# Kernel optimization log

Measured on AMD Instinct MI355X. Metric: run time of the kernel, lower is better.

Reference implementation:

```python
import jax, jax.numpy as jnp
import numpy as np

A, B, S, ADIM = 8, 8192, 128, 16   # n_agents, batch, state_dim, act_dim
H, HEADS = 512, 4                   # hidc, att_heads
D = H // HEADS                      # att_dim
EPS = 1e-5


def _ln(x):
    # LayerNorm over last dim, no affine (elementwise_affine=False), eps=1e-5
    m = jnp.mean(x, axis=-1, keepdims=True)
    v = jnp.var(x, axis=-1, keepdims=True)
    return (x - m) * jax.lax.rsqrt(v + EPS)


def setup_inputs() -> dict:
    key = jax.random.key(0)
    ks = jax.random.split(key, 16)
    sc = 0.02
    return {
        "states": jax.random.normal(ks[0], (A, B, S), jnp.float32),
        "actions": jax.random.normal(ks[1], (A, B, ADIM), jnp.float32),
        # per-agent state encoders (Encoder built with hidc in the source)
        "Ws_s": jax.random.normal(ks[2], (A, S, H), jnp.float32) * sc,
        "bs_s": jnp.zeros((A, H), jnp.float32),
        # per-agent state-action encoders
        "Ws_sa": jax.random.normal(ks[3], (A, S + ADIM, H), jnp.float32) * sc,
        "bs_sa": jnp.zeros((A, H), jnp.float32),
        # shared per-head key/value/selector projections
        "Wk": jax.random.normal(ks[4], (HEADS, H, D), jnp.float32) * sc,
        "Wv": jax.random.normal(ks[5], (HEADS, H, D), jnp.float32) * sc,
        "Wsel": jax.random.normal(ks[6], (HEADS, H, D), jnp.float32) * sc,
        "bsel": jnp.zeros((HEADS, D), jnp.float32),
        # per-agent critics: Linear(2H -> H), LeakyReLU, Linear(H -> ADIM)
        "Wc1": jax.random.normal(ks[7], (A, 2 * H, H), jnp.float32) * sc,
        "bc1": jnp.zeros((A, H), jnp.float32),
        "Wc2": jax.random.normal(ks[8], (A, H, ADIM), jnp.float32) * sc,
        "bc2": jnp.zeros((A, ADIM), jnp.float32),
    }


def reference(states, actions, Ws_s, bs_s, Ws_sa, bs_sa,
              Wk, Wv, Wsel, bsel, Wc1, bc1, Wc2, bc2):
    lrelu = jax.nn.leaky_relu  # slope 0.01 matches torch default

    # per-agent state encodings: [A,B,H]
    s_enc = lrelu(jnp.einsum('abs,ash->abh', _ln(states), Ws_s) + bs_s[:, None, :])

    # per-agent state-action encodings: [A,B,H]
    sa = jnp.concatenate([states, actions], axis=-1)
    sa_enc = lrelu(jnp.einsum('abs,ash->abh', _ln(sa), Ws_sa) + bs_sa[:, None, :])

    # per-head keys / values / selectors: [HEADS, A, B, D]
    keys = jnp.einsum('abh,khd->kabd', sa_enc, Wk)
    vals = jnp.einsum('abh,khd->kabd', sa_enc, Wv)
    sel = lrelu(jnp.einsum('abh,khd->kabd', sa_enc, Wsel) + bsel[:, None, None, :])

    # attention logits of agent i over agents j != i: [HEADS, A, A, B]
    logits = jnp.einsum('kibd,kjbd->kijb', sel, keys) / np.sqrt(D).astype(np.float32)
    self_mask = jnp.eye(A, dtype=bool)[None, :, :, None]
    w = jax.nn.softmax(jnp.where(self_mask, -jnp.inf, logits), axis=2)

    # attended values: [HEADS, A, B, D] -> concat heads -> [A, B, H]
    qvals = jnp.einsum('kijb,kjbd->kibd', w, vals)
    values = qvals.transpose(1, 2, 0, 3).reshape(A, B, H)

    # per-agent critics on concat(state_enc, attended values)
    cin = jnp.concatenate([s_enc, values], axis=-1)           # [A,B,2H]
    h1 = lrelu(jnp.einsum('abf,afh->abh', _ln(cin), Wc1) + bc1[:, None, :])
    all_qs = jnp.einsum('abh,aho->abo', h1, Wc2) + bc2[:, None, :]  # [A,B,ADIM]

    # Q of taken (argmax) action per agent: [A,B,1]
    idx = jnp.argmax(actions, axis=-1)
    q = jnp.take_along_axis(all_qs, idx[..., None], axis=-1)
    return q
```

## Files before the change

### kernel.cpp

```cpp
#include <hip/hip_runtime.h>
#include <hip/hip_bf16.h>
#include <math.h>


#define AN 8
#define BNB 8192
#define SN 128
#define ADN 16
#define HN 512
#define NHEADS 4
#define DN 128

typedef __hip_bfloat16 bf16;
typedef unsigned short u16;
typedef __attribute__((ext_vector_type(8))) short bf16x8;
typedef __attribute__((ext_vector_type(4))) float f32x4;

__device__ __forceinline__ float lrelu(float x){ return x > 0.f ? x : 0.01f*x; }
__device__ __forceinline__ float bflo(unsigned u){ return __uint_as_float(u << 16); }
__device__ __forceinline__ float bfhi(unsigned u){ return __uint_as_float(u & 0xffff0000u); }
__device__ __forceinline__ float bf2f(u16 u){ return __uint_as_float((unsigned)u << 16); }
__device__ __forceinline__ u16 f2bf(float v){
  union { bf16 h; u16 s; } cv; cv.h = __float2bfloat16(v); return cv.s;
}
__device__ __forceinline__ ushort4 f4bf(float4 v){
  ushort4 u; u.x=f2bf(v.x); u.y=f2bf(v.y); u.z=f2bf(v.z); u.w=f2bf(v.w); return u;
}

__device__ __forceinline__ void gload16(const u16* g, u16* l){
  __builtin_amdgcn_global_load_lds(
      (const __attribute__((address_space(1))) unsigned int*)(g),
      (__attribute__((address_space(3))) unsigned int*)(l), 16, 0, 0);
}

__global__ __launch_bounds__(256) void prep_kernel(
    const float* __restrict__ states, const float* __restrict__ actions,
    u16* __restrict__ sa_bf, float2* __restrict__ st_s, float2* __restrict__ st_sa,
    int* __restrict__ aip)
{
  const int lane = threadIdx.x & 63;
  const int r = blockIdx.x*4 + (threadIdx.x >> 6);
  float2 sv = ((const float2*)(states + (size_t)r*SN))[lane];
  float s1 = sv.x + sv.y, q1 = sv.x*sv.x + sv.y*sv.y;
  float2 av = make_float2(0.f, 0.f);
  if (lane < 8) av = ((const float2*)(actions + (size_t)r*ADN))[lane];
  float s2 = s1 + av.x + av.y, q2 = q1 + av.x*av.x + av.y*av.y;
  #pragma unroll
  for (int off=32; off; off>>=1){
    s1 += __shfl_xor(s1,off); q1 += __shfl_xor(q1,off);
    s2 += __shfl_xor(s2,off); q2 += __shfl_xor(q2,off);
  }
  float bv; int bi;
  if (lane < 8){
    if (av.x >= av.y){ bv = av.x; bi = 2*lane; } else { bv = av.y; bi = 2*lane+1; }
  } else { bv = -INFINITY; bi = 999; }
  #pragma unroll
  for (int off=1; off<8; off<<=1){
    float ov = __shfl_xor(bv, off); int oi = __shfl_xor(bi, off);
    if (ov > bv || (ov == bv && oi < bi)){ bv = ov; bi = oi; }
  }
  u16* row = sa_bf + (size_t)r*192;
  ushort2 p; p.x = f2bf(sv.x); p.y = f2bf(sv.y);
  *(ushort2*)(row + 2*lane) = p;
  if (lane < 8){
    ushort2 pa; pa.x = f2bf(av.x); pa.y = f2bf(av.y);
    *(ushort2*)(row + 128 + 2*lane) = pa;
  } else if (lane < 32){
    ushort2 z; z.x = 0; z.y = 0;
    *(ushort2*)(row + 128 + 2*lane) = z;
  }
  if (lane==0){
    float m1 = s1*(1.f/128.f), v1 = fmaxf(q1*(1.f/128.f)-m1*m1, 0.f);
    st_s[r] = make_float2(m1, rsqrtf(v1+1e-5f));
    float m2 = s2*(1.f/144.f), v2 = fmaxf(q2*(1.f/144.f)-m2*m2, 0.f);
    st_sa[r] = make_float2(m2, rsqrtf(v2+1e-5f));
    aip[r] = bi;
  }
}

__global__ __launch_bounds__(256) void transw_all_kernel(
    const float* __restrict__ Ws_s, const float* __restrict__ Ws_sa, const float* __restrict__ Wc1,
    const float* __restrict__ Wk, const float* __restrict__ Wv, const float* __restrict__ Wsel,
    u16* __restrict__ Wt_s, u16* __restrict__ Wt_sa, u16* __restrict__ Wt_c1, u16* __restrict__ Wt_p)
{
  __shared__ float t[32][33];
  int id = blockIdx.x;
  const float* in; u16* outp; int K, Kp; size_t zs; int gx;
  const int N = (id < 5376) ? 512 : 128;
  if (id < 512){            in=Ws_s;  outp=Wt_s;            K=128;  Kp=128;  zs=(size_t)512*128;  gx=4;  }
  else if (id < 1280){ id-=512;  in=Ws_sa; outp=Wt_sa;      K=144;  Kp=192;  zs=(size_t)512*192;  gx=6;  }
  else if (id < 5376){ id-=1280; in=Wc1;   outp=Wt_c1;      K=1024; Kp=1024; zs=(size_t)512*1024; gx=32; }
  else if (id < 5632){ id-=5376; in=Wk;    outp=Wt_p;            K=512; Kp=512; zs=(size_t)3*128*512; gx=16; }
  else if (id < 5888){ id-=5632; in=Wv;    outp=Wt_p+128*512;    K=512; Kp=512; zs=(size_t)3*128*512; gx=16; }
  else {               id-=5888; in=Wsel;  outp=Wt_p+2*128*512;  K=512; Kp=512; zs=(size_t)3*128*512; gx=16; }
  const int bx = id % gx; id /= gx;
  const int gy = N >> 5;
  const int by = id % gy;
  const int z  = id / gy;
  const int tx = threadIdx.x, ty = threadIdx.y;
  const int k0 = bx*32, n0 = by*32;
  const float* ip = in + (size_t)z*K*N;
  #pragma unroll
  for (int i=0;i<4;i++){
    int k = k0 + ty*4 + i;
    t[ty*4+i][tx] = (k < K) ? ip[(size_t)k*N + n0 + tx] : 0.f;
  }
  __syncthreads();
  u16* op = outp + (size_t)z*zs;
  #pragma unroll
  for (int i=0;i<4;i++){
    int n = n0 + ty*4 + i;
    op[(size_t)n*Kp + k0 + tx] = f2bf(t[tx][ty*4+i]);
  }
}

__global__ __launch_bounds__(256) void colsum_bf_kernel(
    const u16* __restrict__ Wt_s, const u16* __restrict__ Wt_sa, const u16* __restrict__ Wt_c1,
    float* __restrict__ cs_s, float* __restrict__ cs_sa, float* __restrict__ cs_c1)
{
  const int lane = threadIdx.x & 63;
  const int row = blockIdx.x*4 + (threadIdx.x >> 6);
  const int which = row >> 12; const int idx = row & 4095;
  const u16* W; int K; float* outp;
  if (which==0){ W = Wt_s;  K = 128;  outp = cs_s;  }
  else if (which==1){ W = Wt_sa; K = 192;  outp = cs_sa; }
  else { W = Wt_c1; K = 1024; outp = cs_c1; }
  const u16* p = W + (size_t)idx*K;
  float s = 0.f;
  for (int c = lane*8; c < K; c += 512){
    uint4 v = *(const uint4*)(p + c);
    const unsigned w4[4] = {v.x, v.y, v.z, v.w};
    #pragma unroll
    for (int t=0;t<4;t++) s += bflo(w4[t]) + bfhi(w4[t]);
  }
  #pragma unroll
  for (int off=32; off; off>>=1) s += __shfl_xor(s,off);
  if (lane==0) outp[idx] = s;
}

template<int MODE>
__global__ __launch_bounds__(256) void mfma_enc_kernel(
    const u16* __restrict__ Aa, const u16* __restrict__ Ab,
    const u16* __restrict__ Wt, const float* __restrict__ bias,
    const float2* __restrict__ stats, const float* __restrict__ csum,
    u16* __restrict__ outp,
    const float* __restrict__ Wc2, const float* __restrict__ bc2,
    const int* __restrict__ aip, float* __restrict__ qout)
{
  constexpr int K   = (MODE==0) ? 128 : (MODE==1 ? 192 : 1024);
  constexpr int LDA = (MODE==2) ? 512 : 192;
  constexpr int KP  = K;
  constexpr int SMEMN = (MODE==2) ? 20736 : 17408;
  __shared__ __align__(16) u16 smem[SMEMN];
  u16* As = smem;
  u16* Bs = smem + 8192;
  const int tid = threadIdx.x;
  const int w = tid>>6, lane = tid&63;
  const int wr = w>>1, wc = w&1;
  const int srow = lane>>3, skq = (lane&7)^srow;

  const int nwg = gridDim.x * gridDim.y;
  int id = blockIdx.y * gridDim.x + blockIdx.x;
  int swz = (id & 7) * (nwg >> 3) + (id >> 3);
  const int bx = swz % gridDim.x, by = swz / gridDim.x;

  const int m0 = by*128, n0c = bx*128;
  const int a = by >> 6;
  const u16* Wbase = Wt + (size_t)a*HN*KP;
  const int slotbase = (lane>>4) ^ (lane&7);
  f32x4 acc[4][4] = {};

  float* wc2l = nullptr; int* ail = nullptr;
  if constexpr (MODE==2){
    wc2l = (float*)(smem + 16384);
    ail  = (int*)(smem + 16384 + 4096);
    for (int e = tid; e < 2048; e += 256){
      const int aidx = e >> 7, col = e & 127;
      wc2l[e] = Wc2[((size_t)a*HN + n0c + col)*ADN + aidx];
    }
    if (tid < 128) ail[tid] = aip[m0 + tid];
  }

  for (int k0 = 0; k0 < K; k0 += 64){
    __syncthreads();
    const u16* asrc; int acol;
    if (MODE==2){ asrc = (k0 < 512) ? Aa : Ab; acol = k0 & 511; }
    else        { asrc = Aa; acol = k0; }
    #pragma unroll
    for (int t=0;t<4;t++){
      const int rr = w*32 + t*8;
      gload16(asrc  + (size_t)(m0  + rr + srow)*LDA + acol + skq*8, As + rr*64);
      gload16(Wbase + (size_t)(n0c + rr + srow)*KP  + k0   + skq*8, Bs + rr*64);
    }
    __syncthreads();
    #pragma unroll
    for (int ks=0; ks<2; ++ks){
      bf16x8 af[4], bv[4];
      const int so = ((slotbase ^ (ks<<2)))*8;
      #pragma unroll
      for (int mi=0;mi<4;mi++) af[mi] = *(const bf16x8*)&As[(wr*64+mi*16+(lane&15))*64 + so];
      #pragma unroll
      for (int ni=0;ni<4;ni++) bv[ni] = *(const bf16x8*)&Bs[(wc*64+ni*16+(lane&15))*64 + so];
      #pragma unroll
      for (int mi=0;mi<4;mi++)
        #pragma unroll
        for (int ni=0;ni<4;ni++)
          acc[mi][ni] = __builtin_amdgcn_mfma_f32_16x16x32_bf16(af[mi], bv[ni], acc[mi][ni], 0, 0, 0);
    }
  }

  __syncthreads();
  float csv[4], biv[4];
  #pragma unroll
  for (int ni=0;ni<4;ni++){
    const int col = n0c + wc*64 + ni*16 + (lane&15);
    csv[ni] = csum[a*HN + col];
    biv[ni] = bias[a*HN + col];
  }

  if constexpr (MODE==2){
    #pragma unroll
    for (int mi=0;mi<4;mi++){
      const int rbase = wr*64 + mi*16 + ((lane>>4)<<2);
      #pragma unroll
      for (int v=0; v<4; ++v){
        const int rl = rbase + v;
        const float2 st = stats[m0 + rl];
        const int aidx = ail[rl];
        float p = 0.f;
        #pragma unroll
        for (int ni=0;ni<4;ni++){
          const int coll = wc*64 + ni*16 + (lane&15);
          const float o = lrelu(st.y*(acc[mi][ni][v] - st.x*csv[ni]) + biv[ni]);
          p = fmaf(o, wc2l[aidx*128 + coll], p);
        }
        p += __shfl_xor(p,1); p += __shfl_xor(p,2);
        p += __shfl_xor(p,4); p += __shfl_xor(p,8);
        if ((lane&15)==0){
          if (n0c==0 && wc==0) p += bc2[a*ADN + aidx];
          atomicAdd(qout + m0 + rl, p);
        }
      }
    }
  } else {
    #pragma unroll
    for (int mi=0;mi<4;mi++){
      const int rl = wr*64 + mi*16 + ((lane>>4)<<2);
      #pragma unroll
      for (int v=0; v<4; ++v){
        const float2 st = stats[m0 + rl + v];
        #pragma unroll
        for (int ni=0;ni<4;ni++){
          const float o = lrelu(st.y*(acc[mi][ni][v] - st.x*csv[ni]) + biv[ni]);
          smem[(rl+v)*136 + wc*64 + ni*16 + (lane&15)] = f2bf(o);
        }
      }
    }
    __syncthreads();
    #pragma unroll
    for (int it=0; it<8; ++it){
      const int rl = it*16 + (tid>>4);
      const int ck = (tid&15)*8;
      const uint4 vv = *(const uint4*)&smem[rl*136 + ck];
      *(uint4*)(outp + (size_t)(m0+rl)*HN + n0c + ck) = vv;
    }
  }
}

__global__ __launch_bounds__(256) void mfma_proj_kernel(
    const u16* __restrict__ sa_enc, const u16* __restrict__ Wt_p,
    const float* __restrict__ bsel, u16* __restrict__ kvs, int head)
{
  __shared__ __align__(16) u16 smem[17408];
  u16* As = smem;
  u16* Bs = smem + 8192;
  const int tid = threadIdx.x;
  const int w = tid>>6, lane = tid&63;
  const int wr = w>>1, wc = w&1;
  const int srow = lane>>3, skq = (lane&7)^srow;

  const int nwg = gridDim.x * gridDim.y;
  int id = blockIdx.y * gridDim.x + blockIdx.x;
  int swz = (id & 7) * (nwg >> 3) + (id >> 3);
  const int t = swz % gridDim.x;
  const int m0 = (swz / gridDim.x) * 128;

  const u16* Wbase = Wt_p + (size_t)(head*3 + t)*DN*HN;
  const int slotbase = (lane>>4) ^ (lane&7);
  f32x4 acc[4][4] = {};

  for (int k0 = 0; k0 < HN; k0 += 64){
    __syncthreads();
    #pragma unroll
    for (int tt=0;tt<4;tt++){
      const int rr = w*32 + tt*8;
      gload16(sa_enc + (size_t)(m0 + rr + srow)*HN + k0 + skq*8, As + rr*64);
      gload16(Wbase  + (size_t)(rr + srow)*HN      + k0 + skq*8, Bs + rr*64);
    }
    __syncthreads();
    #pragma unroll
    for (int ks=0; ks<2; ++ks){
      bf16x8 af[4], bv[4];
      const int so = ((slotbase ^ (ks<<2)))*8;
      #pragma unroll
      for (int mi=0;mi<4;mi++) af[mi] = *(const bf16x8*)&As[(wr*64+mi*16+(lane&15))*64 + so];
      #pragma unroll
      for (int ni=0;ni<4;ni++) bv[ni] = *(const bf16x8*)&Bs[(wc*64+ni*16+(lane&15))*64 + so];
      #pragma unroll
      for (int mi=0;mi<4;mi++)
        #pragma unroll
        for (int ni=0;ni<4;ni++)
          acc[mi][ni] = __builtin_amdgcn_mfma_f32_16x16x32_bf16(af[mi], bv[ni], acc[mi][ni], 0, 0, 0);
    }
  }

  __syncthreads();
  const bool issel = (t == 2);
  float biv[4];
  #pragma unroll
  for (int ni=0;ni<4;ni++){
    const int col = wc*64 + ni*16 + (lane&15);
    biv[ni] = issel ? bsel[head*DN + col] : 0.f;
  }
  #pragma unroll
  for (int mi=0;mi<4;mi++){
    const int rl = wr*64 + mi*16 + ((lane>>4)<<2);
    #pragma unroll
    for (int v=0; v<4; ++v){
      #pragma unroll
      for (int ni=0;ni<4;ni++){
        float o = acc[mi][ni][v] + biv[ni];
        if (issel) o = lrelu(o);
        smem[(rl+v)*136 + wc*64 + ni*16 + (lane&15)] = f2bf(o);
      }
    }
  }
  __syncthreads();
  #pragma unroll
  for (int it=0; it<8; ++it){
    const int rl = it*16 + (tid>>4);
    const int ck = (tid&15)*8;
    const int r = m0 + rl;
    const int ar = r >> 13, b = r & (BNB-1);
    const uint4 vv = *(const uint4*)&smem[rl*136 + ck];
    *(uint4*)(kvs + (((size_t)t*BNB + b)*AN + ar)*DN + ck) = vv;
  }
}

__global__ __launch_bounds__(256) void attn_kernel(
    const u16* __restrict__ kvs, u16* __restrict__ values, int kh)
{
  __shared__ float lds[4][3232];
  const int lane = threadIdx.x & 63;
  const int wv   = threadIdx.x >> 6;
  float* selL = &lds[wv][0];
  float* keyL = &lds[wv][1056];
  float* valL = &lds[wv][2112];
  float* wL   = &lds[wv][3168];
  const int b = blockIdx.x*4 + wv;

  #pragma unroll
  for (int m=0;m<3;m++){
    const int t = (m==0) ? 2 : ((m==1) ? 0 : 1);
    float* dst = (m==0) ? selL : ((m==1) ? keyL : valL);
    const uint2* p = (const uint2*)(kvs + ((size_t)t*BNB + b)*(AN*DN));
    #pragma unroll
    for (int it=0; it<4; it++){
      uint2 u = p[it*64 + lane];
      int e = (it*64 + lane)*4;
      int j = e >> 7, d = e & 127;
      float4 f;
      f.x = bflo(u.x); f.y = bfhi(u.x); f.z = bflo(u.y); f.w = bfhi(u.y);
      *(float4*)&dst[j*132 + d] = f;
    }
  }
  __syncthreads();

  const int i = lane >> 3, j = lane & 7;
  float acc = 0.f;
  #pragma unroll 8
  for (int dq=0; dq<32; dq++){
    const float4 s4 = *(const float4*)&selL[i*132 + dq*4];
    const float4 k4 = *(const float4*)&keyL[j*132 + dq*4];
    acc += s4.x*k4.x + s4.y*k4.y + s4.z*k4.z + s4.w*k4.w;
  }
  float logit = acc * 0.08838834764831845f;
  if (i == j) logit = -INFINITY;
  float mx = logit;
  mx = fmaxf(mx, __shfl_xor(mx,1,8));
  mx = fmaxf(mx, __shfl_xor(mx,2,8));
  mx = fmaxf(mx, __shfl_xor(mx,4,8));
  const float e = __expf(logit - mx);
  float s = e;
  s += __shfl_xor(s,1,8);
  s += __shfl_xor(s,2,8);
  s += __shfl_xor(s,4,8);
  wL[i*8 + j] = e / s;
  __syncthreads();

  const int dq = lane & 7;
  float4 o[4];
  #pragma unroll
  for (int tt=0;tt<4;tt++) o[tt] = make_float4(0.f,0.f,0.f,0.f);
  #pragma unroll
  for (int jj=0;jj<8;jj++){
    const float wj = wL[i*8 + jj];
    #pragma unroll
    for (int tt=0;tt<4;tt++){
      const float4 v4 = *(const float4*)&valL[jj*132 + tt*32 + dq*4];
      o[tt].x += wj*v4.x; o[tt].y += wj*v4.y; o[tt].z += wj*v4.z; o[tt].w += wj*v4.w;
    }
  }
  u16* dst = values + ((size_t)i*BNB + b)*HN + kh*DN;
  #pragma unroll
  for (int tt=0;tt<4;tt++)
    *(ushort4*)(dst + tt*32 + dq*4) = f4bf(o[tt]);
}

__global__ __launch_bounds__(256) void stats_cin_kernel(
    const u16* __restrict__ s_enc, const u16* __restrict__ values, float2* __restrict__ st)
{
  const int lane = threadIdx.x & 63;
  const int r = blockIdx.x*4 + (threadIdx.x >> 6);
  const uint4* p1 = (const uint4*)(s_enc + (size_t)r*HN);
  const uint4* p2 = (const uint4*)(values + (size_t)r*HN);
  uint4 va = p1[lane];
  uint4 vb = p2[lane];
  float s=0.f, q=0.f;
  const unsigned wa[4] = {va.x, va.y, va.z, va.w};
  const unsigned wb[4] = {vb.x, vb.y, vb.z, vb.w};
  #pragma unroll
  for (int t=0;t<4;t++){
    float f0 = bflo(wa[t]), f1 = bfhi(wa[t]);
    float g0 = bflo(wb[t]), g1 = bfhi(wb[t]);
    s += f0+f1+g0+g1; q += f0*f0+f1*f1+g0*g0+g1*g1;
  }
  #pragma unroll
  for (int off=32; off; off>>=1){ s += __shfl_xor(s,off); q += __shfl_xor(q,off); }
  if (lane==0){
    float m = s*(1.f/1024.f); float v = fmaxf(q*(1.f/1024.f) - m*m, 0.f);
    st[r] = make_float2(m, rsqrtf(v + 1e-5f));
  }
}

extern "C" void kernel_launch(void* const* d_in, const int* in_sizes, int n_in,
                              void* d_out, int out_size, void* d_ws, size_t ws_size,
                              hipStream_t stream)
{
  (void)in_sizes; (void)n_in; (void)ws_size;
  const float* states  = (const float*)d_in[0];
  const float* actions = (const float*)d_in[1];
  const float* Ws_s    = (const float*)d_in[2];
  const float* bs_s    = (const float*)d_in[3];
  const float* Ws_sa   = (const float*)d_in[4];
  const float* bs_sa   = (const float*)d_in[5];
  const float* Wk      = (const float*)d_in[6];
  const float* Wv      = (const float*)d_in[7];
  const float* Wsel    = (const float*)d_in[8];
  const float* bsel    = (const float*)d_in[9];
  const float* Wc1     = (const float*)d_in[10];
  const float* bc1     = (const float*)d_in[11];
  const float* Wc2     = (const float*)d_in[12];
  const float* bc2     = (const float*)d_in[13];
  float* outp = (float*)d_out;

  char* ws = (char*)d_ws;
  size_t off = 0;
  auto alloc = [&](size_t n){ void* p = ws + off; off += (n + 255) & ~(size_t)255; return p; };
  u16*    slot1  = (u16*)   alloc((size_t)AN*BNB*HN*2);
  u16*    s_enc  = slot1;
  u16*    kvs    = slot1;
  u16*    sa_enc = (u16*)   alloc((size_t)AN*BNB*HN*2);
  u16*    values = (u16*)   alloc((size_t)AN*BNB*HN*2);
  u16*    sa_bf  = (u16*)   alloc((size_t)AN*BNB*192*2);
  u16*    Wt_s   = (u16*)   alloc((size_t)AN*HN*128*2);
  u16*    Wt_sa  = (u16*)   alloc((size_t)AN*HN*192*2);
  u16*    Wt_c1  = (u16*)   alloc((size_t)AN*HN*1024*2);
  u16*    Wt_p   = (u16*)   alloc((size_t)NHEADS*3*DN*HN*2);
  float2* st_s   = (float2*)alloc((size_t)AN*BNB*8);
  float2* st_sa  = (float2*)alloc((size_t)AN*BNB*8);
  float2* st_cin = (float2*)alloc((size_t)AN*BNB*8);
  float*  cs_s   = (float*) alloc((size_t)AN*HN*4);
  float*  cs_sa  = (float*) alloc((size_t)AN*HN*4);
  float*  cs_c1  = (float*) alloc((size_t)AN*HN*4);
  int*    aip    = (int*)   alloc((size_t)AN*BNB*4);

  hipMemsetAsync(d_out, 0, (size_t)out_size*4, stream);
  prep_kernel<<<dim3(AN*BNB/4), 256, 0, stream>>>(states, actions, sa_bf, st_s, st_sa, aip);
  transw_all_kernel<<<dim3(6144), dim3(32,8), 0, stream>>>(
      Ws_s, Ws_sa, Wc1, Wk, Wv, Wsel, Wt_s, Wt_sa, Wt_c1, Wt_p);
  colsum_bf_kernel<<<dim3(3*AN*HN/4), 256, 0, stream>>>(Wt_s, Wt_sa, Wt_c1, cs_s, cs_sa, cs_c1);

  mfma_enc_kernel<1><<<dim3(4,512), 256, 0, stream>>>(sa_bf, nullptr, Wt_sa, bs_sa, st_sa, cs_sa,
                                                      sa_enc, nullptr, nullptr, nullptr, nullptr);
  for (int kh = 0; kh < NHEADS; ++kh){
    mfma_proj_kernel<<<dim3(3,512), 256, 0, stream>>>(sa_enc, Wt_p, bsel, kvs, kh);
    attn_kernel<<<dim3(BNB/4), 256, 0, stream>>>(kvs, values, kh);
  }
  mfma_enc_kernel<0><<<dim3(4,512), 256, 0, stream>>>(sa_bf, nullptr, Wt_s, bs_s, st_s, cs_s,
                                                      s_enc, nullptr, nullptr, nullptr, nullptr);
  stats_cin_kernel<<<dim3(AN*BNB/4), 256, 0, stream>>>(s_enc, values, st_cin);
  mfma_enc_kernel<2><<<dim3(4,512), 256, 0, stream>>>(s_enc, values, Wt_c1, bc1, st_cin, cs_c1,
                                                      nullptr, Wc2, bc2, aip, outp);
}
```

Baseline: 471.7 us.

## Fuse per-head key/value/selector projection with attention in one kernel

Replaces the per-head loop of projection GEMM plus attention kernels (8 launches) with one kernel per 8-batch tile. Each block keeps its 64 sa_enc rows in registers as A fragments, computes K, V and selector for every head into LDS, then runs the masked softmax attention and writes values directly. This removes the global round trip of the kvs intermediate and the repeated sa_enc reloads. In exchange each block streams all projection weights through LDS with only 64 rows of M, so weight reuse per block is lower. It uses 64KB of LDS and a large register footprint, which may limit occupancy.

After: 619.8 us. 31.4% more time.

```diff
diff --git a/kernel.cpp b/kernel.cpp
--- a/kernel.cpp
+++ b/kernel.cpp
@@ -22,6 +22,9 @@
 __device__ __forceinline__ float bf2f(u16 u){ return __uint_as_float((unsigned)u << 16); }
 __device__ __forceinline__ u16 f2bf(float v){
   union { bf16 h; u16 s; } cv; cv.h = __float2bfloat16(v); return cv.s;
+}
+__device__ __forceinline__ unsigned pk2(float a, float b){
+  return (unsigned)f2bf(a) | ((unsigned)f2bf(b) << 16);
 }
 __device__ __forceinline__ ushort4 f4bf(float4 v){
   ushort4 u; u.x=f2bf(v.x); u.y=f2bf(v.y); u.z=f2bf(v.z); u.w=f2bf(v.w); return u;
@@ -267,154 +270,136 @@
   }
 }
 
-__global__ __launch_bounds__(256) void mfma_proj_kernel(
+__global__ __launch_bounds__(256) void fused_pa_kernel(
     const u16* __restrict__ sa_enc, const u16* __restrict__ Wt_p,
-    const float* __restrict__ bsel, u16* __restrict__ kvs, int head)
-{
-  __shared__ __align__(16) u16 smem[17408];
-  u16* As = smem;
-  u16* Bs = smem + 8192;
+    const float* __restrict__ bsel, u16* __restrict__ values)
+{
+  __shared__ __align__(16) u16 smem[32768];
+  u16* Bst  = smem;
+  u16* bufK = smem + 8192;
+  u16* bufV = smem + 16384;
+  u16* bufS = smem + 24576;
   const int tid = threadIdx.x;
-  const int w = tid>>6, lane = tid&63;
-  const int wr = w>>1, wc = w&1;
-  const int srow = lane>>3, skq = (lane&7)^srow;
-
-  const int nwg = gridDim.x * gridDim.y;
-  int id = blockIdx.y * gridDim.x + blockIdx.x;
-  int swz = (id & 7) * (nwg >> 3) + (id >> 3);
-  const int t = swz % gridDim.x;
-  const int m0 = (swz / gridDim.x) * 128;
-
-  const u16* Wbase = Wt_p + (size_t)(head*3 + t)*DN*HN;
-  const int slotbase = (lane>>4) ^ (lane&7);
-  f32x4 acc[4][4] = {};
-
-  for (int k0 = 0; k0 < HN; k0 += 64){
+  const int w = tid >> 6, lane = tid & 63;
+  const int b0 = blockIdx.x * 8;
+  const int srow = lane >> 3, skq = (lane & 7) ^ srow;
+  const int slotbase = (lane >> 4) ^ (lane & 7);
+
+  bf16x8 af[16];
+  {
+    const int tr = lane & 15;
+    const int rr = w*16 + tr;
+    const u16* arow = sa_enc + ((size_t)(rr>>3)*BNB + b0 + (rr&7))*HN + (lane>>4)*8;
+    #pragma unroll
+    for (int kc = 0; kc < 16; ++kc)
+      af[kc] = *(const bf16x8*)(arow + kc*32);
+  }
+
+  for (int h = 0; h < NHEADS; ++h){
+    for (int t = 0; t < 3; ++t){
+      const u16* Wb = Wt_p + (size_t)(h*3 + t)*DN*HN;
+      f32x4 acc[8] = {};
+      #pragma unroll
+      for (int kc64 = 0; kc64 < 8; ++kc64){
+        __syncthreads();
+        #pragma unroll
+        for (int tt = 0; tt < 4; ++tt){
+          const int rb = w*32 + tt*8;
+          gload16(Wb + (size_t)(rb + srow)*HN + kc64*64 + skq*8, Bst + rb*64);
+        }
+        __syncthreads();
+        #pragma unroll
+        for (int ks = 0; ks < 2; ++ks){
+          const int so = (slotbase ^ (ks << 2)) * 8;
+          bf16x8 bv[8];
+          #pragma unroll
+          for (int ni = 0; ni < 8; ++ni)
+            bv[ni] = *(const bf16x8*)&Bst[(ni*16 + (lane & 15))*64 + so];
+          #pragma unroll
+          for (int ni = 0; ni < 8; ++ni)
+            acc[ni] = __builtin_amdgcn_mfma_f32_16x16x32_bf16(af[kc64*2+ks], bv[ni], acc[ni], 0, 0, 0);
+        }
+      }
+      u16* obuf = (t==0) ? bufK : (t==1) ? bufV : bufS;
+      float bsl[8];
+      if (t == 2){
+        #pragma unroll
+        for (int ni = 0; ni < 8; ++ni) bsl[ni] = bsel[h*DN + ni*16 + (lane&15)];
+      }
+      #pragma unroll
+      for (int ni = 0; ni < 8; ++ni){
+        #pragma unroll
+        for (int v = 0; v < 4; ++v){
+          const int rr2 = w*16 + ((lane>>4)<<2) + v;
+          float o = acc[ni][v];
+          if (t == 2) o = lrelu(o + bsl[ni]);
+          int idx = rr2*128 + ni*16 + (lane & 15);
+          idx ^= ((rr2 >> 3) & 7) << 3;
+          obuf[idx] = f2bf(o);
+        }
+      }
+    }
     __syncthreads();
-    #pragma unroll
-    for (int tt=0;tt<4;tt++){
-      const int rr = w*32 + tt*8;
-      gload16(sa_enc + (size_t)(m0 + rr + srow)*HN + k0 + skq*8, As + rr*64);
-      gload16(Wbase  + (size_t)(rr + srow)*HN      + k0 + skq*8, Bs + rr*64);
+
+    #pragma unroll
+    for (int bb = 0; bb < 2; ++bb){
+      const int i = w*2 + bb;
+      const int ai = lane >> 3, aj = lane & 7;
+      float dot = 0.f;
+      #pragma unroll
+      for (int s = 0; s < 16; ++s){
+        const int sidx = (ai*8 + i)*128 + ((s ^ ai) & 15)*8;
+        const int kidx = (aj*8 + i)*128 + ((s ^ aj) & 15)*8;
+        uint4 sv = *(const uint4*)&bufS[sidx];
+        uint4 kv = *(const uint4*)&bufK[kidx];
+        dot += bflo(sv.x)*bflo(kv.x) + bfhi(sv.x)*bfhi(kv.x);
+        dot += bflo(sv.y)*bflo(kv.y) + bfhi(sv.y)*bfhi(kv.y);
+        dot += bflo(sv.z)*bflo(kv.z) + bfhi(sv.z)*bfhi(kv.z);
+        dot += bflo(sv.w)*bflo(kv.w) + bfhi(sv.w)*bfhi(kv.w);
+      }
+      float logit = dot * 0.08838834764831845f;
+      if (ai == aj) logit = -INFINITY;
+      float mx = logit;
+      mx = fmaxf(mx, __shfl_xor(mx,1,8));
+      mx = fmaxf(mx, __shfl_xor(mx,2,8));
+      mx = fmaxf(mx, __shfl_xor(mx,4,8));
+      const float e = __expf(logit - mx);
+      float ssum = e;
+      ssum += __shfl_xor(ssum,1,8);
+      ssum += __shfl_xor(ssum,2,8);
+      ssum += __shfl_xor(ssum,4,8);
+      const float wgt = e / ssum;
+
+      const int dc = lane & 7;
+      float o[16];
+      #pragma unroll
+      for (int q = 0; q < 16; ++q) o[q] = 0.f;
+      #pragma unroll
+      for (int j = 0; j < 8; ++j){
+        const float wj = __shfl(wgt, j, 8);
+        const int vrow = (j*8 + i)*128;
+        const uint4 v0 = *(const uint4*)&bufV[vrow + (((dc*2)   ^ j) & 15)*8];
+        const uint4 v1 = *(const uint4*)&bufV[vrow + (((dc*2+1) ^ j) & 15)*8];
+        o[0]  += wj*bflo(v0.x); o[1]  += wj*bfhi(v0.x);
+        o[2]  += wj*bflo(v0.y); o[3]  += wj*bfhi(v0.y);
+        o[4]  += wj*bflo(v0.z); o[5]  += wj*bfhi(v0.z);
+        o[6]  += wj*bflo(v0.w); o[7]  += wj*bfhi(v0.w);
+        o[8]  += wj*bflo(v1.x); o[9]  += wj*bfhi(v1.x);
+        o[10] += wj*bflo(v1.y); o[11] += wj*bfhi(v1.y);
+        o[12] += wj*bflo(v1.z); o[13] += wj*bfhi(v1.z);
+        o[14] += wj*bflo(v1.w); o[15] += wj*bfhi(v1.w);
+      }
+      uint4 p0, p1;
+      p0.x = pk2(o[0],o[1]);   p0.y = pk2(o[2],o[3]);
+      p0.z = pk2(o[4],o[5]);   p0.w = pk2(o[6],o[7]);
+      p1.x = pk2(o[8],o[9]);   p1.y = pk2(o[10],o[11]);
+      p1.z = pk2(o[12],o[13]); p1.w = pk2(o[14],o[15]);
+      u16* dst = values + ((size_t)ai*BNB + b0 + i)*HN + h*DN + dc*16;
+      *(uint4*)dst = p0;
+      *(uint4*)(dst + 8) = p1;
     }
     __syncthreads();
-    #pragma unroll
-    for (int ks=0; ks<2; ++ks){
-      bf16x8 af[4], bv[4];
-      const int so = ((slotbase ^ (ks<<2)))*8;
-      #pragma unroll
-      for (int mi=0;mi<4;mi++) af[mi] = *(const bf16x8*)&As[(wr*64+mi*16+(lane&15))*64 + so];
-      #pragma unroll
-      for (int ni=0;ni<4;ni++) bv[ni] = *(const bf16x8*)&Bs[(wc*64+ni*16+(lane&15))*64 + so];
-      #pragma unroll
-      for (int mi=0;mi<4;mi++)
-        #pragma unroll
-        for (int ni=0;ni<4;ni++)
-          acc[mi][ni] = __builtin_amdgcn_mfma_f32_16x16x32_bf16(af[mi], bv[ni], acc[mi][ni], 0, 0, 0);
-    }
-  }
-
-  __syncthreads();
-  const bool issel = (t == 2);
-  float biv[4];
-  #pragma unroll
-  for (int ni=0;ni<4;ni++){
-    const int col = wc*64 + ni*16 + (lane&15);
-    biv[ni] = issel ? bsel[head*DN + col] : 0.f;
-  }
-  #pragma unroll
-  for (int mi=0;mi<4;mi++){
-    const int rl = wr*64 + mi*16 + ((lane>>4)<<2);
-    #pragma unroll
-    for (int v=0; v<4; ++v){
-      #pragma unroll
-      for (int ni=0;ni<4;ni++){
-        float o = acc[mi][ni][v] + biv[ni];
-        if (issel) o = lrelu(o);
-        smem[(rl+v)*136 + wc*64 + ni*16 + (lane&15)] = f2bf(o);
-      }
-    }
-  }
-  __syncthreads();
-  #pragma unroll
-  for (int it=0; it<8; ++it){
-    const int rl = it*16 + (tid>>4);
-    const int ck = (tid&15)*8;
-    const int r = m0 + rl;
-    const int ar = r >> 13, b = r & (BNB-1);
-    const uint4 vv = *(const uint4*)&smem[rl*136 + ck];
-    *(uint4*)(kvs + (((size_t)t*BNB + b)*AN + ar)*DN + ck) = vv;
-  }
-}
-
-__global__ __launch_bounds__(256) void attn_kernel(
-    const u16* __restrict__ kvs, u16* __restrict__ values, int kh)
-{
-  __shared__ float lds[4][3232];
-  const int lane = threadIdx.x & 63;
-  const int wv   = threadIdx.x >> 6;
-  float* selL = &lds[wv][0];
-  float* keyL = &lds[wv][1056];
-  float* valL = &lds[wv][2112];
-  float* wL   = &lds[wv][3168];
-  const int b = blockIdx.x*4 + wv;
-
-  #pragma unroll
-  for (int m=0;m<3;m++){
-    const int t = (m==0) ? 2 : ((m==1) ? 0 : 1);
-    float* dst = (m==0) ? selL : ((m==1) ? keyL : valL);
-    const uint2* p = (const uint2*)(kvs + ((size_t)t*BNB + b)*(AN*DN));
-    #pragma unroll
-    for (int it=0; it<4; it++){
-      uint2 u = p[it*64 + lane];
-      int e = (it*64 + lane)*4;
-      int j = e >> 7, d = e & 127;
-      float4 f;
-      f.x = bflo(u.x); f.y = bfhi(u.x); f.z = bflo(u.y); f.w = bfhi(u.y);
-      *(float4*)&dst[j*132 + d] = f;
-    }
-  }
-  __syncthreads();
-
-  const int i = lane >> 3, j = lane & 7;
-  float acc = 0.f;
-  #pragma unroll 8
-  for (int dq=0; dq<32; dq++){
-    const float4 s4 = *(const float4*)&selL[i*132 + dq*4];
-    const float4 k4 = *(const float4*)&keyL[j*132 + dq*4];
-    acc += s4.x*k4.x + s4.y*k4.y + s4.z*k4.z + s4.w*k4.w;
-  }
-  float logit = acc * 0.08838834764831845f;
-  if (i == j) logit = -INFINITY;
-  float mx = logit;
-  mx = fmaxf(mx, __shfl_xor(mx,1,8));
-  mx = fmaxf(mx, __shfl_xor(mx,2,8));
-  mx = fmaxf(mx, __shfl_xor(mx,4,8));
-  const float e = __expf(logit - mx);
-  float s = e;
-  s += __shfl_xor(s,1,8);
-  s += __shfl_xor(s,2,8);
-  s += __shfl_xor(s,4,8);
-  wL[i*8 + j] = e / s;
-  __syncthreads();
-
-  const int dq = lane & 7;
-  float4 o[4];
-  #pragma unroll
-  for (int tt=0;tt<4;tt++) o[tt] = make_float4(0.f,0.f,0.f,0.f);
-  #pragma unroll
-  for (int jj=0;jj<8;jj++){
-    const float wj = wL[i*8 + jj];
-    #pragma unroll
-    for (int tt=0;tt<4;tt++){
-      const float4 v4 = *(const float4*)&valL[jj*132 + tt*32 + dq*4];
-      o[tt].x += wj*v4.x; o[tt].y += wj*v4.y; o[tt].z += wj*v4.z; o[tt].w += wj*v4.w;
-    }
-  }
-  u16* dst = values + ((size_t)i*BNB + b)*HN + kh*DN;
-  #pragma unroll
-  for (int tt=0;tt<4;tt++)
-    *(ushort4*)(dst + tt*32 + dq*4) = f4bf(o[tt]);
+  }
 }
 
 __global__ __launch_bounds__(256) void stats_cin_kernel(
@@ -467,9 +452,7 @@
   char* ws = (char*)d_ws;
   size_t off = 0;
   auto alloc = [&](size_t n){ void* p = ws + off; off += (n + 255) & ~(size_t)255; return p; };
-  u16*    slot1  = (u16*)   alloc((size_t)AN*BNB*HN*2);
-  u16*    s_enc  = slot1;
-  u16*    kvs    = slot1;
+  u16*    s_enc  = (u16*)   alloc((size_t)AN*BNB*HN*2);
   u16*    sa_enc = (u16*)   alloc((size_t)AN*BNB*HN*2);
   u16*    values = (u16*)   alloc((size_t)AN*BNB*HN*2);
   u16*    sa_bf  = (u16*)   alloc((size_t)AN*BNB*192*2);
@@ -493,12 +476,9 @@
 
   mfma_enc_kernel<1><<<dim3(4,512), 256, 0, stream>>>(sa_bf, nullptr, Wt_sa, bs_sa, st_sa, cs_sa,
                                                       sa_enc, nullptr, nullptr, nullptr, nullptr);
-  for (int kh = 0; kh < NHEADS; ++kh){
-    mfma_proj_kernel<<<dim3(3,512), 256, 0, stream>>>(sa_enc, Wt_p, bsel, kvs, kh);
-    attn_kernel<<<dim3(BNB/4), 256, 0, stream>>>(kvs, values, kh);
-  }
   mfma_enc_kernel<0><<<dim3(4,512), 256, 0, stream>>>(sa_bf, nullptr, Wt_s, bs_s, st_s, cs_s,
                                                       s_enc, nullptr, nullptr, nullptr, nullptr);
+  fused_pa_kernel<<<dim3(BNB/8), 256, 0, stream>>>(sa_enc, Wt_p, bsel, values);
   stats_cin_kernel<<<dim3(AN*BNB/4), 256, 0, stream>>>(s_enc, values, st_cin);
   mfma_enc_kernel<2><<<dim3(4,512), 256, 0, stream>>>(s_enc, values, Wt_c1, bc1, st_cin, cs_c1,
                                                       nullptr, Wc2, bc2, aip, outp);
```

## Fuse critic LayerNorm statistics into encoder and attention epilogues via atomics

Applied to the files above, without the earlier changes.

Removes the separate stats_cin kernel that re-read s_enc and values to compute per-row mean and variance for the critic LayerNorm. The epilogues of the state encoder and of the attention kernel now accumulate each row's sum and sum of squares with atomics into a zeroed buffer. The critic kernel then derives mean and rstd from those sums. This saves a full pass over about 128 MB of bf16 data, at the cost of many float atomics and a memset. Statistics are now taken from fp32 values before bf16 rounding, which slightly changes numerics.

Measured after the change: 523.0 us. +10.9%, slower.

```diff
diff --git a/kernel.cpp b/kernel.cpp
--- a/kernel.cpp
+++ b/kernel.cpp
@@ -143,7 +143,7 @@
     const u16* __restrict__ Aa, const u16* __restrict__ Ab,
     const u16* __restrict__ Wt, const float* __restrict__ bias,
     const float2* __restrict__ stats, const float* __restrict__ csum,
-    u16* __restrict__ outp,
+    u16* __restrict__ outp, float2* __restrict__ stacc,
     const float* __restrict__ Wc2, const float* __restrict__ bc2,
     const int* __restrict__ aip, float* __restrict__ qout)
 {
@@ -225,13 +225,15 @@
       #pragma unroll
       for (int v=0; v<4; ++v){
         const int rl = rbase + v;
-        const float2 st = stats[m0 + rl];
+        const float2 sq = stats[m0 + rl];
+        const float mn = sq.x*(1.f/1024.f);
+        const float rstd = rsqrtf(fmaxf(sq.y*(1.f/1024.f) - mn*mn, 0.f) + 1e-5f);
         const int aidx = ail[rl];
         float p = 0.f;
         #pragma unroll
         for (int ni=0;ni<4;ni++){
           const int coll = wc*64 + ni*16 + (lane&15);
-          const float o = lrelu(st.y*(acc[mi][ni][v] - st.x*csv[ni]) + biv[ni]);
+          const float o = lrelu(rstd*(acc[mi][ni][v] - mn*csv[ni]) + biv[ni]);
           p = fmaf(o, wc2l[aidx*128 + coll], p);
         }
         p += __shfl_xor(p,1); p += __shfl_xor(p,2);
@@ -249,10 +251,22 @@
       #pragma unroll
       for (int v=0; v<4; ++v){
         const float2 st = stats[m0 + rl + v];
+        float rs = 0.f, rq = 0.f;
         #pragma unroll
         for (int ni=0;ni<4;ni++){
           const float o = lrelu(st.y*(acc[mi][ni][v] - st.x*csv[ni]) + biv[ni]);
           smem[(rl+v)*136 + wc*64 + ni*16 + (lane&15)] = f2bf(o);
+          rs += o; rq += o*o;
+        }
+        if constexpr (MODE==0){
+          rs += __shfl_xor(rs,1); rq += __shfl_xor(rq,1);
+          rs += __shfl_xor(rs,2); rq += __shfl_xor(rq,2);
+          rs += __shfl_xor(rs,4); rq += __shfl_xor(rq,4);
+          rs += __shfl_xor(rs,8); rq += __shfl_xor(rq,8);
+          if ((lane&15)==0){
+            float* sa = (float*)(stacc + m0 + rl + v);
+            atomicAdd(sa, rs); atomicAdd(sa+1, rq);
+          }
         }
       }
     }
@@ -348,7 +362,7 @@
 }
 
 __global__ __launch_bounds__(256) void attn_kernel(
-    const u16* __restrict__ kvs, u16* __restrict__ values, int kh)
+    const u16* __restrict__ kvs, u16* __restrict__ values, float2* __restrict__ stacc, int kh)
 {
   __shared__ float lds[4][3232];
   const int lane = threadIdx.x & 63;
@@ -415,31 +429,19 @@
   #pragma unroll
   for (int tt=0;tt<4;tt++)
     *(ushort4*)(dst + tt*32 + dq*4) = f4bf(o[tt]);
-}
-
-__global__ __launch_bounds__(256) void stats_cin_kernel(
-    const u16* __restrict__ s_enc, const u16* __restrict__ values, float2* __restrict__ st)
-{
-  const int lane = threadIdx.x & 63;
-  const int r = blockIdx.x*4 + (threadIdx.x >> 6);
-  const uint4* p1 = (const uint4*)(s_enc + (size_t)r*HN);
-  const uint4* p2 = (const uint4*)(values + (size_t)r*HN);
-  uint4 va = p1[lane];
-  uint4 vb = p2[lane];
-  float s=0.f, q=0.f;
-  const unsigned wa[4] = {va.x, va.y, va.z, va.w};
-  const unsigned wb[4] = {vb.x, vb.y, vb.z, vb.w};
-  #pragma unroll
-  for (int t=0;t<4;t++){
-    float f0 = bflo(wa[t]), f1 = bfhi(wa[t]);
-    float g0 = bflo(wb[t]), g1 = bfhi(wb[t]);
-    s += f0+f1+g0+g1; q += f0*f0+f1*f1+g0*g0+g1*g1;
-  }
-  #pragma unroll
-  for (int off=32; off; off>>=1){ s += __shfl_xor(s,off); q += __shfl_xor(q,off); }
-  if (lane==0){
-    float m = s*(1.f/1024.f); float v = fmaxf(q*(1.f/1024.f) - m*m, 0.f);
-    st[r] = make_float2(m, rsqrtf(v + 1e-5f));
+
+  float rs = 0.f, rq = 0.f;
+  #pragma unroll
+  for (int tt=0;tt<4;tt++){
+    rs += o[tt].x + o[tt].y + o[tt].z + o[tt].w;
+    rq += o[tt].x*o[tt].x + o[tt].y*o[tt].y + o[tt].z*o[tt].z + o[tt].w*o[tt].w;
+  }
+  rs += __shfl_xor(rs,1,8); rq += __shfl_xor(rq,1,8);
+  rs += __shfl_xor(rs,2,8); rq += __shfl_xor(rq,2,8);
+  rs += __shfl_xor(rs,4,8); rq += __shfl_xor(rq,4,8);
+  if (dq == 0){
+    float* sa = (float*)(stacc + (size_t)i*BNB + b);
+    atomicAdd(sa, rs); atomicAdd(sa + 1, rq);
   }
 }
 
@@ -486,20 +488,20 @@
   int*    aip    = (int*)   alloc((size_t)AN*BNB*4);
 
   hipMemsetAsync(d_out, 0, (size_t)out_size*4, stream);
+  hipMemsetAsync(st_cin, 0, (size_t)AN*BNB*8, stream);
   prep_kernel<<<dim3(AN*BNB/4), 256, 0, stream>>>(states, actions, sa_bf, st_s, st_sa, aip);
   transw_all_kernel<<<dim3(6144), dim3(32,8), 0, stream>>>(
       Ws_s, Ws_sa, Wc1, Wk, Wv, Wsel, Wt_s, Wt_sa, Wt_c1, Wt_p);
   colsum_bf_kernel<<<dim3(3*AN*HN/4), 256, 0, stream>>>(Wt_s, Wt_sa, Wt_c1, cs_s, cs_sa, cs_c1);
 
   mfma_enc_kernel<1><<<dim3(4,512), 256, 0, stream>>>(sa_bf, nullptr, Wt_sa, bs_sa, st_sa, cs_sa,
-                                                      sa_enc, nullptr, nullptr, nullptr, nullptr);
+                                                      sa_enc, nullptr, nullptr, nullptr, nullptr, nullptr);
   for (int kh = 0; kh < NHEADS; ++kh){
     mfma_proj_kernel<<<dim3(3,512), 256, 0, stream>>>(sa_enc, Wt_p, bsel, kvs, kh);
-    attn_kernel<<<dim3(BNB/4), 256, 0, stream>>>(kvs, values, kh);
+    attn_kernel<<<dim3(BNB/4), 256, 0, stream>>>(kvs, values, st_cin, kh);
   }
   mfma_enc_kernel<0><<<dim3(4,512), 256, 0, stream>>>(sa_bf, nullptr, Wt_s, bs_s, st_s, cs_s,
-                                                      s_enc, nullptr, nullptr, nullptr, nullptr);
-  stats_cin_kernel<<<dim3(AN*BNB/4), 256, 0, stream>>>(s_enc, values, st_cin);
+                                                      s_enc, st_cin, nullptr, nullptr, nullptr, nullptr);
   mfma_enc_kernel<2><<<dim3(4,512), 256, 0, stream>>>(s_enc, values, Wt_c1, bc1, st_cin, cs_c1,
-                                                      nullptr, Wc2, bc2, aip, outp);
-}
+                                                      nullptr, nullptr, Wc2, bc2, aip, outp);
+}
```

## Replace critic GEMM with 256x256-tile double-buffered pipelined MFMA kernel

Applied to the files above, without the earlier changes.

Splits the critic-layer GEMM (K=1024) out of the generic encoder kernel into a dedicated kernel. It uses 512 threads, 256x256 output tiles, and double-buffered LDS staging with async global loads interleaved between MFMA phases, plus explicit waitcnt, barriers and setprio. The aim is to hide global-load latency and raise arithmetic intensity on the largest GEMM, which the single-buffered 128x128 version left exposed. The larger LDS footprint (~148KB) and higher register pressure limit occupancy, and the hand scheduling is fragile.

Result: faster. 460.9 us (-2.3%).

```diff
diff --git a/kernel.cpp b/kernel.cpp
--- a/kernel.cpp
+++ b/kernel.cpp
@@ -140,18 +140,15 @@
 
 template<int MODE>
 __global__ __launch_bounds__(256) void mfma_enc_kernel(
-    const u16* __restrict__ Aa, const u16* __restrict__ Ab,
+    const u16* __restrict__ Aa,
     const u16* __restrict__ Wt, const float* __restrict__ bias,
     const float2* __restrict__ stats, const float* __restrict__ csum,
-    u16* __restrict__ outp,
-    const float* __restrict__ Wc2, const float* __restrict__ bc2,
-    const int* __restrict__ aip, float* __restrict__ qout)
-{
-  constexpr int K   = (MODE==0) ? 128 : (MODE==1 ? 192 : 1024);
-  constexpr int LDA = (MODE==2) ? 512 : 192;
+    u16* __restrict__ outp)
+{
+  constexpr int K   = (MODE==0) ? 128 : 192;
+  constexpr int LDA = 192;
   constexpr int KP  = K;
-  constexpr int SMEMN = (MODE==2) ? 20736 : 17408;
-  __shared__ __align__(16) u16 smem[SMEMN];
+  __shared__ __align__(16) u16 smem[17408];
   u16* As = smem;
   u16* Bs = smem + 8192;
   const int tid = threadIdx.x;
@@ -170,27 +167,13 @@
   const int slotbase = (lane>>4) ^ (lane&7);
   f32x4 acc[4][4] = {};
 
-  float* wc2l = nullptr; int* ail = nullptr;
-  if constexpr (MODE==2){
-    wc2l = (float*)(smem + 16384);
-    ail  = (int*)(smem + 16384 + 4096);
-    for (int e = tid; e < 2048; e += 256){
-      const int aidx = e >> 7, col = e & 127;
-      wc2l[e] = Wc2[((size_t)a*HN + n0c + col)*ADN + aidx];
-    }
-    if (tid < 128) ail[tid] = aip[m0 + tid];
-  }
-
   for (int k0 = 0; k0 < K; k0 += 64){
     __syncthreads();
-    const u16* asrc; int acol;
-    if (MODE==2){ asrc = (k0 < 512) ? Aa : Ab; acol = k0 & 511; }
-    else        { asrc = Aa; acol = k0; }
     #pragma unroll
     for (int t=0;t<4;t++){
       const int rr = w*32 + t*8;
-      gload16(asrc  + (size_t)(m0  + rr + srow)*LDA + acol + skq*8, As + rr*64);
-      gload16(Wbase + (size_t)(n0c + rr + srow)*KP  + k0   + skq*8, Bs + rr*64);
+      gload16(Aa    + (size_t)(m0  + rr + srow)*LDA + k0 + skq*8, As + rr*64);
+      gload16(Wbase + (size_t)(n0c + rr + srow)*KP  + k0 + skq*8, Bs + rr*64);
     }
     __syncthreads();
     #pragma unroll
@@ -217,52 +200,202 @@
     csv[ni] = csum[a*HN + col];
     biv[ni] = bias[a*HN + col];
   }
-
-  if constexpr (MODE==2){
-    #pragma unroll
-    for (int mi=0;mi<4;mi++){
-      const int rbase = wr*64 + mi*16 + ((lane>>4)<<2);
-      #pragma unroll
-      for (int v=0; v<4; ++v){
-        const int rl = rbase + v;
-        const float2 st = stats[m0 + rl];
-        const int aidx = ail[rl];
-        float p = 0.f;
-        #pragma unroll
-        for (int ni=0;ni<4;ni++){
-          const int coll = wc*64 + ni*16 + (lane&15);
-          const float o = lrelu(st.y*(acc[mi][ni][v] - st.x*csv[ni]) + biv[ni]);
-          p = fmaf(o, wc2l[aidx*128 + coll], p);
-        }
-        p += __shfl_xor(p,1); p += __shfl_xor(p,2);
-        p += __shfl_xor(p,4); p += __shfl_xor(p,8);
-        if ((lane&15)==0){
-          if (n0c==0 && wc==0) p += bc2[a*ADN + aidx];
-          atomicAdd(qout + m0 + rl, p);
-        }
-      }
-    }
-  } else {
-    #pragma unroll
-    for (int mi=0;mi<4;mi++){
-      const int rl = wr*64 + mi*16 + ((lane>>4)<<2);
-      #pragma unroll
-      for (int v=0; v<4; ++v){
-        const float2 st = stats[m0 + rl + v];
-        #pragma unroll
-        for (int ni=0;ni<4;ni++){
-          const float o = lrelu(st.y*(acc[mi][ni][v] - st.x*csv[ni]) + biv[ni]);
-          smem[(rl+v)*136 + wc*64 + ni*16 + (lane&15)] = f2bf(o);
-        }
-      }
-    }
-    __syncthreads();
-    #pragma unroll
-    for (int it=0; it<8; ++it){
-      const int rl = it*16 + (tid>>4);
-      const int ck = (tid&15)*8;
-      const uint4 vv = *(const uint4*)&smem[rl*136 + ck];
-      *(uint4*)(outp + (size_t)(m0+rl)*HN + n0c + ck) = vv;
+  #pragma unroll
+  for (int mi=0;mi<4;mi++){
+    const int rl = wr*64 + mi*16 + ((lane>>4)<<2);
+    #pragma unroll
+    for (int v=0; v<4; ++v){
+      const float2 st = stats[m0 + rl + v];
+      #pragma unroll
+      for (int ni=0;ni<4;ni++){
+        const float o = lrelu(st.y*(acc[mi][ni][v] - st.x*csv[ni]) + biv[ni]);
+        smem[(rl+v)*136 + wc*64 + ni*16 + (lane&15)] = f2bf(o);
+      }
+    }
+  }
+  __syncthreads();
+  #pragma unroll
+  for (int it=0; it<8; ++it){
+    const int rl = it*16 + (tid>>4);
+    const int ck = (tid&15)*8;
+    const uint4 vv = *(const uint4*)&smem[rl*136 + ck];
+    *(uint4*)(outp + (size_t)(m0+rl)*HN + n0c + ck) = vv;
+  }
+}
+
+__global__ __launch_bounds__(512, 2) void mfma_critic_kernel(
+    const u16* __restrict__ Aa, const u16* __restrict__ Ab,
+    const u16* __restrict__ Wt, const float* __restrict__ bias,
+    const float2* __restrict__ stats, const float* __restrict__ csum,
+    const float* __restrict__ Wc2, const float* __restrict__ bc2,
+    const int* __restrict__ aip, float* __restrict__ qout)
+{
+  __shared__ __align__(16) u16 smem[74240];
+  const int tid = threadIdx.x;
+  const int w = tid >> 6, lane = tid & 63;
+  const int wr = w >> 2, wc = w & 3;
+  const int srow = lane >> 3, skq = (lane & 7) ^ srow;
+  const int slotx = lane >> 4, lanx = lane & 7, lr = lane & 15;
+
+  const int nwg = gridDim.x * gridDim.y;
+  int id = blockIdx.y * gridDim.x + blockIdx.x;
+  int swz = (id & 7) * (nwg >> 3) + (id >> 3);
+  const int bx = swz % gridDim.x, by = swz / gridDim.x;
+  const int m0 = by * 256, n0c = bx * 256;
+  const int a = m0 >> 13;
+  const u16* Wbase = Wt + (size_t)a * HN * 1024;
+
+  float* wc2l = (float*)(smem + 65536);
+  int*   ail  = (int*)(smem + 65536 + 8192);
+  #pragma unroll
+  for (int i = 0; i < 8; ++i){
+    const int e = i*512 + tid;
+    const int aidx = e >> 8, col = e & 255;
+    wc2l[e] = Wc2[((size_t)a*HN + n0c + col)*ADN + aidx];
+  }
+  if (tid < 256) ail[tid] = aip[m0 + tid];
+
+  auto STAGE = [&](int tau, int part){
+    u16* dst = smem + (tau & 1)*32768 + ((part >> 1) ? 16384 : 0) + (part & 1)*8192 + w*1024;
+    if (part < 2){
+      const int k0 = tau * 64;
+      const u16* asrc = (k0 < 512) ? Aa : Ab;
+      const int acol = (k0 & 511) + skq*8;
+      const int grow = m0 + (part & 1)*128 + w*16 + srow;
+      gload16(asrc + (size_t)grow*HN + acol, dst);
+      gload16(asrc + (size_t)(grow + 8)*HN + acol, dst + 512);
+    } else {
+      const int bcol = tau*64 + skq*8;
+      const int grow = n0c + (part & 1)*128 + w*16 + srow;
+      gload16(Wbase + (size_t)grow*1024 + bcol, dst);
+      gload16(Wbase + (size_t)(grow + 8)*1024 + bcol, dst + 512);
+    }
+  };
+
+  STAGE(0,0); STAGE(0,1); STAGE(0,2); STAGE(0,3);
+  STAGE(1,0); STAGE(1,1); STAGE(1,2); STAGE(1,3);
+  asm volatile("s_waitcnt vmcnt(8)" ::: "memory");
+  __builtin_amdgcn_sched_barrier(0);
+  __builtin_amdgcn_s_barrier();
+
+  f32x4 acc[8][4] = {};
+
+  #pragma unroll 1
+  for (int tau = 0; tau < 16; ++tau){
+    const u16* AB = smem + (tau & 1)*32768;
+    const int so0 = ((0 | slotx) ^ lanx)*8;
+    const int so1 = ((4 | slotx) ^ lanx)*8;
+    bf16x8 af[4][2], bn01[2][2], bn23[2][2];
+
+    #pragma unroll
+    for (int mf = 0; mf < 4; ++mf){
+      const int r = (wr*128 + mf*16 + lr)*64;
+      af[mf][0] = *(const bf16x8*)&AB[r + so0];
+      af[mf][1] = *(const bf16x8*)&AB[r + so1];
+    }
+    #pragma unroll
+    for (int nf = 0; nf < 2; ++nf){
+      const int r = 16384 + (wc*64 + nf*16 + lr)*64;
+      bn01[nf][0] = *(const bf16x8*)&AB[r + so0];
+      bn01[nf][1] = *(const bf16x8*)&AB[r + so1];
+    }
+    if (tau >= 1 && tau <= 14) STAGE(tau + 1, 0);
+    __builtin_amdgcn_s_barrier();
+    __builtin_amdgcn_s_setprio(1);
+    #pragma unroll
+    for (int mf = 0; mf < 4; ++mf)
+      #pragma unroll
+      for (int nf = 0; nf < 2; ++nf){
+        acc[mf][nf] = __builtin_amdgcn_mfma_f32_16x16x32_bf16(af[mf][0], bn01[nf][0], acc[mf][nf], 0,0,0);
+        acc[mf][nf] = __builtin_amdgcn_mfma_f32_16x16x32_bf16(af[mf][1], bn01[nf][1], acc[mf][nf], 0,0,0);
+      }
+    __builtin_amdgcn_s_setprio(0);
+    __builtin_amdgcn_s_barrier();
+
+    #pragma unroll
+    for (int nf = 0; nf < 2; ++nf){
+      const int r = 16384 + (wc*64 + (nf + 2)*16 + lr)*64;
+      bn23[nf][0] = *(const bf16x8*)&AB[r + so0];
+      bn23[nf][1] = *(const bf16x8*)&AB[r + so1];
+    }
+    if (tau >= 1 && tau <= 14) STAGE(tau + 1, 1);
+    __builtin_amdgcn_s_barrier();
+    __builtin_amdgcn_s_setprio(1);
+    #pragma unroll
+    for (int mf = 0; mf < 4; ++mf)
+      #pragma unroll
+      for (int nf = 0; nf < 2; ++nf){
+        acc[mf][nf+2] = __builtin_amdgcn_mfma_f32_16x16x32_bf16(af[mf][0], bn23[nf][0], acc[mf][nf+2], 0,0,0);
+        acc[mf][nf+2] = __builtin_amdgcn_mfma_f32_16x16x32_bf16(af[mf][1], bn23[nf][1], acc[mf][nf+2], 0,0,0);
+      }
+    __builtin_amdgcn_s_setprio(0);
+    __builtin_amdgcn_s_barrier();
+
+    #pragma unroll
+    for (int mf = 0; mf < 4; ++mf){
+      const int r = (wr*128 + (mf + 4)*16 + lr)*64;
+      af[mf][0] = *(const bf16x8*)&AB[r + so0];
+      af[mf][1] = *(const bf16x8*)&AB[r + so1];
+    }
+    if (tau <= 13) STAGE(tau + 2, 2);
+    __builtin_amdgcn_s_barrier();
+    __builtin_amdgcn_s_setprio(1);
+    #pragma unroll
+    for (int mf = 0; mf < 4; ++mf)
+      #pragma unroll
+      for (int nf = 0; nf < 2; ++nf){
+        acc[mf+4][nf+2] = __builtin_amdgcn_mfma_f32_16x16x32_bf16(af[mf][0], bn23[nf][0], acc[mf+4][nf+2], 0,0,0);
+        acc[mf+4][nf+2] = __builtin_amdgcn_mfma_f32_16x16x32_bf16(af[mf][1], bn23[nf][1], acc[mf+4][nf+2], 0,0,0);
+      }
+    __builtin_amdgcn_s_setprio(0);
+    __builtin_amdgcn_s_barrier();
+
+    if (tau <= 13) STAGE(tau + 2, 3);
+    __builtin_amdgcn_s_barrier();
+    __builtin_amdgcn_s_setprio(1);
+    #pragma unroll
+    for (int mf = 0; mf < 4; ++mf)
+      #pragma unroll
+      for (int nf = 0; nf < 2; ++nf){
+        acc[mf+4][nf] = __builtin_amdgcn_mfma_f32_16x16x32_bf16(af[mf][0], bn01[nf][0], acc[mf+4][nf], 0,0,0);
+        acc[mf+4][nf] = __builtin_amdgcn_mfma_f32_16x16x32_bf16(af[mf][1], bn01[nf][1], acc[mf+4][nf], 0,0,0);
+      }
+    __builtin_amdgcn_s_setprio(0);
+
+    if (tau < 14)       { asm volatile("s_waitcnt vmcnt(4)" ::: "memory"); }
+    else if (tau == 14) { asm volatile("s_waitcnt vmcnt(0)" ::: "memory"); }
+    __builtin_amdgcn_sched_barrier(0);
+    __builtin_amdgcn_s_barrier();
+    __builtin_amdgcn_sched_barrier(0);
+  }
+
+  float csv[4], biv[4];
+  #pragma unroll
+  for (int nf = 0; nf < 4; ++nf){
+    const int col = n0c + wc*64 + nf*16 + lr;
+    csv[nf] = csum[a*HN + col];
+    biv[nf] = bias[a*HN + col];
+  }
+  #pragma unroll
+  for (int mf = 0; mf < 8; ++mf){
+    const int rbase = wr*128 + mf*16 + slotx*4;
+    #pragma unroll
+    for (int v = 0; v < 4; ++v){
+      const int rl = rbase + v;
+      const float2 st = stats[m0 + rl];
+      const int aidx = ail[rl];
+      float p = 0.f;
+      #pragma unroll
+      for (int nf = 0; nf < 4; ++nf){
+        const float o = lrelu(st.y*(acc[mf][nf][v] - st.x*csv[nf]) + biv[nf]);
+        p = fmaf(o, wc2l[aidx*256 + wc*64 + nf*16 + lr], p);
+      }
+      p += __shfl_xor(p,1); p += __shfl_xor(p,2);
+      p += __shfl_xor(p,4); p += __shfl_xor(p,8);
+      if (lr == 0){
+        if (n0c == 0 && wc == 0) p += bc2[a*ADN + aidx];
+        atomicAdd(qout + m0 + rl, p);
+      }
     }
   }
 }
@@ -491,15 +624,13 @@
       Ws_s, Ws_sa, Wc1, Wk, Wv, Wsel, Wt_s, Wt_sa, Wt_c1, Wt_p);
   colsum_bf_kernel<<<dim3(3*AN*HN/4), 256, 0, stream>>>(Wt_s, Wt_sa, Wt_c1, cs_s, cs_sa, cs_c1);
 
-  mfma_enc_kernel<1><<<dim3(4,512), 256, 0, stream>>>(sa_bf, nullptr, Wt_sa, bs_sa, st_sa, cs_sa,
-                                                      sa_enc, nullptr, nullptr, nullptr, nullptr);
+  mfma_enc_kernel<1><<<dim3(4,512), 256, 0, stream>>>(sa_bf, Wt_sa, bs_sa, st_sa, cs_sa, sa_enc);
   for (int kh = 0; kh < NHEADS; ++kh){
     mfma_proj_kernel<<<dim3(3,512), 256, 0, stream>>>(sa_enc, Wt_p, bsel, kvs, kh);
     attn_kernel<<<dim3(BNB/4), 256, 0, stream>>>(kvs, values, kh);
   }
-  mfma_enc_kernel<0><<<dim3(4,512), 256, 0, stream>>>(sa_bf, nullptr, Wt_s, bs_s, st_s, cs_s,
-                                                      s_enc, nullptr, nullptr, nullptr, nullptr);
+  mfma_enc_kernel<0><<<dim3(4,512), 256, 0, stream>>>(sa_bf, Wt_s, bs_s, st_s, cs_s, s_enc);
   stats_cin_kernel<<<dim3(AN*BNB/4), 256, 0, stream>>>(s_enc, values, st_cin);
-  mfma_enc_kernel<2><<<dim3(4,512), 256, 0, stream>>>(s_enc, values, Wt_c1, bc1, st_cin, cs_c1,
-                                                      nullptr, Wc2, bc2, aip, outp);
-}
+  mfma_critic_kernel<<<dim3(2,256), 512, 0, stream>>>(s_enc, values, Wt_c1, bc1, st_cin, cs_c1,
+                                                      Wc2, bc2, aip, outp);
+}
```
